# Performance work log

Measured on AMD Instinct MI355X. Metric: run time of the kernel, lower is better.

## Reference

```python
import jax, jax.numpy as jnp
import numpy as np

B, C, F, H, W = 8, 16, 256, 112, 112   # batch, cells/image, channels, height, width
NB = 3                                  # tgt_shape = (3, 3) adaptive pool bins


def setup_inputs() -> dict:
    key = jax.random.key(0)
    kf, ky, kx, kry, krx, kn = jax.random.split(key, 6)
    feature_maps = jax.random.normal(kf, (B, F, H, W), jnp.float32)
    N = B * C
    # random rectangular cell blobs with bernoulli interior holes + guaranteed core
    cy = jax.random.randint(ky, (N, 1, 1), 20, H - 20)
    cx = jax.random.randint(kx, (N, 1, 1), 20, W - 20)
    ry = jax.random.randint(kry, (N, 1, 1), 5, 18)
    rx = jax.random.randint(krx, (N, 1, 1), 5, 18)
    yy = jnp.arange(H)[None, :, None]
    xx = jnp.arange(W)[None, None, :]
    rect = (jnp.abs(yy - cy) <= ry) & (jnp.abs(xx - cx) <= rx)
    noise = jax.random.bernoulli(kn, 0.8, (N, H, W))
    core = (jnp.abs(yy - cy) <= 2) & (jnp.abs(xx - cx) <= 2)
    cell_masks = rect & (noise | core)            # [N, H, W] bool, each nonempty
    cell_counts = jnp.full((B,), C, jnp.int32)    # fixed cells per image
    return {"feature_maps": feature_maps, "cell_masks": cell_masks,
            "cell_counts": cell_counts}


def _bin_membership(lo, hi, length):
    # adaptive-pool bin i covers [lo + floor(i*sz/NB), lo + ceil((i+1)*sz/NB))
    i = jnp.arange(NB)
    sz = (hi - lo)[..., None]                      # [B, C, 1]
    start = lo[..., None] + (i * sz) // NB         # [B, C, NB]
    end = lo[..., None] + ((i + 1) * sz + NB - 1) // NB
    pos = jnp.arange(length)
    return (pos >= start[..., None]) & (pos < end[..., None])  # [B, C, NB, L]


def reference(feature_maps, cell_masks, cell_counts):
    Bv, Fv, Hv, Wv = feature_maps.shape
    Cv = cell_masks.shape[0] // Bv
    masks = cell_masks.reshape(Bv, Cv, Hv, Wv)
    # tight bbox per cell (first/last True row and column, exclusive end)
    rows = masks.any(-1)                            # [B, C, H]
    cols = masks.any(-2)                            # [B, C, W]
    y0 = jnp.argmax(rows, -1)
    y1 = Hv - jnp.argmax(rows[..., ::-1], -1)
    x0 = jnp.argmax(cols, -1)
    x1 = Wv - jnp.argmax(cols[..., ::-1], -1)
    ymem = _bin_membership(y0, y1, Hv)              # [B, C, NB, H]
    xmem = _bin_membership(x0, x1, Wv)              # [B, C, NB, W]
    neg = jnp.finfo(feature_maps.dtype).min
    feat = feature_maps[:, None]                    # [B, 1, F, H, W]
    m = masks[:, :, None]                           # [B, C, 1, H, W]
    pooled = []
    for i in range(NB):
        ym = ymem[:, :, i][:, :, None, :, None]     # [B, C, 1, H, 1]
        for j in range(NB):
            xm = xmem[:, :, j][:, :, None, None, :]  # [B, C, 1, 1, W]
            inbin = ym & xm
            # inside bin & mask -> feature; inside bin & ~mask -> 0 (zeroed crop);
            # outside bin -> -inf (excluded from max)
            v = jnp.where(inbin & m, feat, jnp.where(inbin, 0.0, neg))
            pooled.append(v.max((-1, -2)))          # [B, C, F]
    out = jnp.stack(pooled, -1)                     # [B, C, F, 9], index = i*NB + j
    # matches torch pooled.view(-1): flatten order f*9 + i*3 + j
    return out.reshape(Bv * Cv, Fv * NB * NB)
```

## Files before the change

### kernel.cpp

```cpp
#include <hip/hip_runtime.h>
#include <float.h>

#define B_  8
#define C_  16
#define N_  (B_*C_)
#define F_  256
#define H_  112
#define W_  112
#define HW_ (H_*W_)
#define NB_ 3

#define FPAR 2
#define WPB  4
#define FPB  (FPAR*WPB)
#define LMS  64


__global__ __launch_bounds__(256) void bbox_kernel(const int4* __restrict__ mask4,
                                                   int* __restrict__ bb) {
    int n = blockIdx.x, t = threadIdx.x;
    const int4* m = mask4 + (size_t)n * (HW_ / 4);
    int ymin = 1 << 20, ymax = -1, xmin = 1 << 20, xmax = -1;
    for (int i = t; i < HW_ / 4; i += 256) {
        int4 v = m[i];
        int y = i / 28;
        int xb = (i - y * 28) * 4;
        if (v.x | v.y | v.z | v.w) { ymin = min(ymin, y); ymax = max(ymax, y); }
        if (v.x) { xmin = min(xmin, xb);     xmax = max(xmax, xb);     }
        if (v.y) { xmin = min(xmin, xb + 1); xmax = max(xmax, xb + 1); }
        if (v.z) { xmin = min(xmin, xb + 2); xmax = max(xmax, xb + 2); }
        if (v.w) { xmin = min(xmin, xb + 3); xmax = max(xmax, xb + 3); }
    }
    #pragma unroll
    for (int off = 32; off; off >>= 1) {
        ymin = min(ymin, __shfl_xor(ymin, off));
        ymax = max(ymax, __shfl_xor(ymax, off));
        xmin = min(xmin, __shfl_xor(xmin, off));
        xmax = max(xmax, __shfl_xor(xmax, off));
    }
    __shared__ int red[4][4];
    int wave = t >> 6;
    if ((t & 63) == 0) {
        red[wave][0] = ymin; red[wave][1] = ymax;
        red[wave][2] = xmin; red[wave][3] = xmax;
    }
    __syncthreads();
    if (t == 0) {
        for (int w = 1; w < 4; ++w) {
            ymin = min(ymin, red[w][0]); ymax = max(ymax, red[w][1]);
            xmin = min(xmin, red[w][2]); xmax = max(xmax, red[w][3]);
        }
        int y0 = ymin, y1 = ymax + 1, x0 = xmin, x1 = xmax + 1;
        int* o = bb + n * 16;
        o[0] = y0; o[1] = y1; o[2] = x0; o[3] = x1;
        int szy = y1 - y0, szx = x1 - x0;
        for (int i = 0; i < NB_; ++i) {
            o[4+i]  = y0 + (i*szy)/NB_;
            o[7+i]  = y0 + ((i+1)*szy + NB_-1)/NB_;
            o[10+i] = x0 + (i*szx)/NB_;
            o[13+i] = x0 + ((i+1)*szx + NB_-1)/NB_;
        }
    }
}

__global__ __launch_bounds__(256) void pool_kernel(
        const float* __restrict__ feat, const int* __restrict__ mask,
        const int* __restrict__ bb, float* __restrict__ out) {
    int n = blockIdx.x;
    int b = n >> 4;
    const int* o = bb + n * 16;
    int y0 = o[0], x0 = o[2];
    int bh = o[1] - y0, bw = o[3] - x0;
    int x0a = x0 & ~3;
    int x1 = x0 + bw;

    __shared__ float lm[37 * LMS];
    {
        const int* mrow = mask + (size_t)n * HW_ + (size_t)y0 * W_ + x0a;
        int tot = bh * (LMS / 4);
        for (int idx = threadIdx.x; idx < tot; idx += 256) {
            int dy = idx >> 4, g = idx & 15;
            int gx = x0a + 4 * g;
            int4 m4 = *(const int4*)(mrow + (size_t)dy * W_ + 4 * g);
            float4 v;
            v.x = (m4.x && gx     >= x0 && gx     < x1) ? 1.f : 0.f;
            v.y = (m4.y && gx + 1 >= x0 && gx + 1 < x1) ? 1.f : 0.f;
            v.z = (m4.z && gx + 2 >= x0 && gx + 2 < x1) ? 1.f : 0.f;
            v.w = (m4.w && gx + 3 >= x0 && gx + 3 < x1) ? 1.f : 0.f;
            *(float4*)(&lm[dy * LMS + 4 * g]) = v;
        }
    }
    __syncthreads();

    int lane = threadIdx.x & 63, wave = threadIdx.x >> 6;
    int xq = lane & 15, rg = lane >> 4;
    int wbw = (x0 - x0a) + bw;
    int xq4 = (4 * xq < wbw) ? 4 * xq : 0;
    int f0 = blockIdx.y * FPB + wave * FPAR;
    const float* gp0 = feat + (size_t)(b * F_ + f0) * HW_ + (size_t)y0 * W_ + x0a + xq4;
    const float* gp1 = gp0 + HW_;

    int ys[3] = {o[4], o[5], o[6]};
    int yem1[3] = {o[7] - 1, o[8] - 1, o[9] - 1};
    int maxlen = max(o[7] - o[4], max(o[8] - o[5], o[9] - o[6]));
    int Tmax = (maxlen + 3) >> 2;

    float acc[3][4][FPAR];
    #pragma unroll
    for (int i = 0; i < 3; ++i)
        #pragma unroll
        for (int s = 0; s < 4; ++s)
            #pragma unroll
            for (int pp = 0; pp < FPAR; ++pp) acc[i][s][pp] = -FLT_MAX;

    for (int t = 0; t < Tmax; ++t) {
        int dy[3];
        #pragma unroll
        for (int i = 0; i < 3; ++i)
            dy[i] = min(ys[i] + 4 * t + rg, yem1[i]) - y0;
        float4 mv[3], c0[3], c1[3];
        #pragma unroll
        for (int i = 0; i < 3; ++i) {
            mv[i] = *(const float4*)(lm + dy[i] * LMS + 4 * xq);
            c0[i] = *(const float4*)(gp0 + dy[i] * W_);
            c1[i] = *(const float4*)(gp1 + dy[i] * W_);
        }
        #pragma unroll
        for (int i = 0; i < 3; ++i) {
            float v0[4] = {mv[i].x*c0[i].x, mv[i].y*c0[i].y, mv[i].z*c0[i].z, mv[i].w*c0[i].w};
            float v1[4] = {mv[i].x*c1[i].x, mv[i].y*c1[i].y, mv[i].z*c1[i].z, mv[i].w*c1[i].w};
            #pragma unroll
            for (int s = 0; s < 4; ++s) {
                acc[i][s][0] = fmaxf(acc[i][s][0], v0[s]);
                acc[i][s][1] = fmaxf(acc[i][s][1], v1[s]);
            }
        }
    }

    int xs[3] = {o[10], o[11], o[12]};
    int xe[3] = {o[13], o[14], o[15]};
    int xg = x0a + 4 * xq;
    #pragma unroll
    for (int pp = 0; pp < FPAR; ++pp) {
        float part[9];
        #pragma unroll
        for (int j = 0; j < 3; ++j) {
            #pragma unroll
            for (int i = 0; i < 3; ++i) {
                float r = -FLT_MAX;
                #pragma unroll
                for (int s = 0; s < 4; ++s) {
                    int xx = xg + s;
                    float lim = (xx >= xs[j] && xx < xe[j]) ? FLT_MAX : -FLT_MAX;
                    r = fmaxf(r, fminf(acc[i][s][pp], lim));
                }
                part[i * 3 + j] = r;
            }
        }
        #pragma unroll
        for (int off = 32; off; off >>= 1)
            #pragma unroll
            for (int q = 0; q < 9; ++q)
                part[q] = fmaxf(part[q], __shfl_xor(part[q], off));
        float st = part[0];
        #pragma unroll
        for (int q = 1; q < 9; ++q) st = (lane == q) ? part[q] : st;
        if (lane < 9) out[(size_t)(n * F_ + f0 + pp) * 9 + lane] = st;
    }
}

extern "C" void kernel_launch(void* const* d_in, const int* in_sizes, int n_in,
                              void* d_out, int out_size, void* d_ws, size_t ws_size,
                              hipStream_t stream) {
    const float* feat = (const float*)d_in[0];
    const int*   mask = (const int*)d_in[1];
    int* bb = (int*)d_ws;

    bbox_kernel<<<N_, 256, 0, stream>>>((const int4*)mask, bb);
    dim3 grid(N_, F_ / FPB);
    pool_kernel<<<grid, 256, 0, stream>>>(feat, mask, bb, (float*)d_out);
}
```

Baseline: 177.4 us.

## Assign one y-bin per lane row-group and widen features per wave

Restructures the pool kernel so each 16-lane row group scans a single vertical adaptive-pool bin row by row, instead of every lane covering all three bins with a stride-4 row step. Each wave now handles four features instead of two, and blocks shrink to 128 threads. This cuts accumulator registers and shortens the cross-lane reduction to 3 values over 16 lanes. In exchange, the fourth row group does redundant work and each thread runs a longer serial loop.

```diff
diff --git a/kernel.cpp b/kernel.cpp
--- a/kernel.cpp
+++ b/kernel.cpp
@@ -10,8 +10,8 @@
 #define HW_ (H_*W_)
 #define NB_ 3
 
-#define FPAR 2
-#define WPB  4
+#define FPAR 4
+#define WPB  2
 #define FPB  (FPAR*WPB)
 #define LMS  64
 
@@ -63,7 +63,7 @@
     }
 }
 
-__global__ __launch_bounds__(256) void pool_kernel(
+__global__ __launch_bounds__(128) void pool_kernel(
         const float* __restrict__ feat, const int* __restrict__ mask,
         const int* __restrict__ bb, float* __restrict__ out) {
     int n = blockIdx.x;
@@ -78,7 +78,7 @@
     {
         const int* mrow = mask + (size_t)n * HW_ + (size_t)y0 * W_ + x0a;
         int tot = bh * (LMS / 4);
-        for (int idx = threadIdx.x; idx < tot; idx += 256) {
+        for (int idx = threadIdx.x; idx < tot; idx += 128) {
             int dy = idx >> 4, g = idx & 15;
             int gx = x0a + 4 * g;
             int4 m4 = *(const int4*)(mrow + (size_t)dy * W_ + 4 * g);
@@ -94,78 +94,71 @@
 
     int lane = threadIdx.x & 63, wave = threadIdx.x >> 6;
     int xq = lane & 15, rg = lane >> 4;
+    int bi = min(rg, 2);
     int wbw = (x0 - x0a) + bw;
     int xq4 = (4 * xq < wbw) ? 4 * xq : 0;
     int f0 = blockIdx.y * FPB + wave * FPAR;
-    const float* gp0 = feat + (size_t)(b * F_ + f0) * HW_ + (size_t)y0 * W_ + x0a + xq4;
-    const float* gp1 = gp0 + HW_;
+    const float* gp = feat + (size_t)(b * F_ + f0) * HW_ + (size_t)y0 * W_ + x0a + xq4;
 
-    int ys[3] = {o[4], o[5], o[6]};
-    int yem1[3] = {o[7] - 1, o[8] - 1, o[9] - 1};
-    int maxlen = max(o[7] - o[4], max(o[8] - o[5], o[9] - o[6]));
-    int Tmax = (maxlen + 3) >> 2;
+    int ysb  = o[4 + bi];
+    int yeb1 = o[7 + bi] - 1;
+    int Tmax = max(o[7] - o[4], max(o[8] - o[5], o[9] - o[6]));
 
-    float acc[3][4][FPAR];
+    float acc[4][FPAR];
     #pragma unroll
-    for (int i = 0; i < 3; ++i)
+    for (int s = 0; s < 4; ++s)
         #pragma unroll
-        for (int s = 0; s < 4; ++s)
-            #pragma unroll
-            for (int pp = 0; pp < FPAR; ++pp) acc[i][s][pp] = -FLT_MAX;
+        for (int pp = 0; pp < FPAR; ++pp) acc[s][pp] = -FLT_MAX;
 
     for (int t = 0; t < Tmax; ++t) {
-        int dy[3];
+        int dy = min(ysb + t, yeb1) - y0;
+        int off = dy * W_;
+        float4 mv = *(const float4*)(lm + dy * LMS + 4 * xq);
+        float4 c[FPAR];
         #pragma unroll
-        for (int i = 0; i < 3; ++i)
-            dy[i] = min(ys[i] + 4 * t + rg, yem1[i]) - y0;
-        float4 mv[3], c0[3], c1[3];
+        for (int pp = 0; pp < FPAR; ++pp)
+            c[pp] = *(const float4*)(gp + (size_t)pp * HW_ + off);
         #pragma unroll
-        for (int i = 0; i < 3; ++i) {
-            mv[i] = *(const float4*)(lm + dy[i] * LMS + 4 * xq);
-            c0[i] = *(const float4*)(gp0 + dy[i] * W_);
-            c1[i] = *(const float4*)(gp1 + dy[i] * W_);
-        }
-        #pragma unroll
-        for (int i = 0; i < 3; ++i) {
-            float v0[4] = {mv[i].x*c0[i].x, mv[i].y*c0[i].y, mv[i].z*c0[i].z, mv[i].w*c0[i].w};
-            float v1[4] = {mv[i].x*c1[i].x, mv[i].y*c1[i].y, mv[i].z*c1[i].z, mv[i].w*c1[i].w};
-            #pragma unroll
-            for (int s = 0; s < 4; ++s) {
-                acc[i][s][0] = fmaxf(acc[i][s][0], v0[s]);
-                acc[i][s][1] = fmaxf(acc[i][s][1], v1[s]);
-            }
+        for (int pp = 0; pp < FPAR; ++pp) {
+            acc[0][pp] = fmaxf(acc[0][pp], mv.x * c[pp].x);
+            acc[1][pp] = fmaxf(acc[1][pp], mv.y * c[pp].y);
+            acc[2][pp] = fmaxf(acc[2][pp], mv.z * c[pp].z);
+            acc[3][pp] = fmaxf(acc[3][pp], mv.w * c[pp].w);
         }
     }
 
-    int xs[3] = {o[10], o[11], o[12]};
-    int xe[3] = {o[13], o[14], o[15]};
     int xg = x0a + 4 * xq;
+    float lim[3][4];
+    #pragma unroll
+    for (int j = 0; j < 3; ++j) {
+        int xs = o[10 + j], xe = o[13 + j];
+        #pragma unroll
+        for (int s = 0; s < 4; ++s) {
+            int xx = xg + s;
+            lim[j][s] = (xx >= xs && xx < xe) ? FLT_MAX : -FLT_MAX;
+        }
+    }
     #pragma unroll
     for (int pp = 0; pp < FPAR; ++pp) {
-        float part[9];
+        float part[3];
         #pragma unroll
         for (int j = 0; j < 3; ++j) {
-            #pragma unroll
-            for (int i = 0; i < 3; ++i) {
-                float r = -FLT_MAX;
-                #pragma unroll
-                for (int s = 0; s < 4; ++s) {
-                    int xx = xg + s;
-                    float lim = (xx >= xs[j] && xx < xe[j]) ? FLT_MAX : -FLT_MAX;
-                    r = fmaxf(r, fminf(acc[i][s][pp], lim));
-                }
-                part[i * 3 + j] = r;
-            }
+            float r = fminf(acc[0][pp], lim[j][0]);
+            r = fmaxf(r, fminf(acc[1][pp], lim[j][1]));
+            r = fmaxf(r, fminf(acc[2][pp], lim[j][2]));
+            r = fmaxf(r, fminf(acc[3][pp], lim[j][3]));
+            part[j] = r;
         }
         #pragma unroll
-        for (int off = 32; off; off >>= 1)
+        for (int off = 1; off <= 8; off <<= 1) {
             #pragma unroll
-            for (int q = 0; q < 9; ++q)
-                part[q] = fmaxf(part[q], __shfl_xor(part[q], off));
-        float st = part[0];
-        #pragma unroll
-        for (int q = 1; q < 9; ++q) st = (lane == q) ? part[q] : st;
-        if (lane < 9) out[(size_t)(n * F_ + f0 + pp) * 9 + lane] = st;
+            for (int j = 0; j < 3; ++j)
+                part[j] = fmaxf(part[j], __shfl_xor(part[j], off));
+        }
+        if (xq == 0 && rg < 3) {
+            float* op = out + (size_t)(n * F_ + f0 + pp) * 9 + rg * 3;
+            op[0] = part[0]; op[1] = part[1]; op[2] = part[2];
+        }
     }
 }
 
@@ -178,5 +171,5 @@
 
     bbox_kernel<<<N_, 256, 0, stream>>>((const int4*)mask, bb);
     dim3 grid(N_, F_ / FPB);
-    pool_kernel<<<grid, 256, 0, stream>>>(feat, mask, bb, (float*)d_out);
+    pool_kernel<<<grid, 128, 0, stream>>>(feat, mask, bb, (float*)d_out);
 }
```

New measurement: 174.8 us. No clear change (-1.5%).
